# Kernel tuning notes

Measured on AMD Instinct MI355X. Metric: run time of the kernel, lower is better.

Reference implementation:

```python
import jax, jax.numpy as jnp
import numpy as np

BN_EPS = 1e-3  # Keras BatchNormalization default epsilon


def _conv_block(x, k):
    """Per-task conv (stride 2, pad 1) -> ReLU -> BatchNorm (center/scale=False, training).

    x: [B, E, H, W, Cin]  (B tasks, E examples per task)
    k: [B, kh, kw, Cin, Cout]  per-task kernel
    """
    def conv_one(xe, kt):  # xe: [E,H,W,Cin], kt: [kh,kw,Cin,Cout]
        return jax.lax.conv_general_dilated(
            xe, kt, window_strides=(2, 2), padding=[(1, 1), (1, 1)],
            dimension_numbers=('NHWC', 'HWIO', 'NHWC'))
    y = jax.nn.relu(jax.vmap(conv_one)(x, k))  # [B,E,H',W',Cout]
    # BatchNorm in training mode: moments over all axes except channels
    m = jnp.mean(y, axis=(0, 1, 2, 3))
    v = jnp.var(y, axis=(0, 1, 2, 3))
    return (y - m) * jax.lax.rsqrt(v + BN_EPS)


def setup_inputs() -> dict:
    key = jax.random.key(0)
    ks = jax.random.split(key, 6)
    B, E, H, C, O = 64, 64, 28, 64, 20
    return {
        'x': jax.random.normal(ks[0], (B, E, H, H, 1), dtype=jnp.float32),
        'k1': jax.random.normal(ks[1], (B, 3, 3, 1, C), dtype=jnp.float32) * 0.1,
        'k2': jax.random.normal(ks[2], (B, 3, 3, C, C), dtype=jnp.float32) * 0.05,
        'k3': jax.random.normal(ks[3], (B, 3, 3, C, C), dtype=jnp.float32) * 0.05,
        'k4': jax.random.normal(ks[4], (B, 3, 3, C, C), dtype=jnp.float32) * 0.05,
        'w_ro': jax.random.normal(ks[5], (B, C, O), dtype=jnp.float32) * 0.1,
    }


def reference(x, k1, k2, k3, k4, w_ro):
    h = _conv_block(x, k1)   # [B,E,14,14,C]
    h = _conv_block(h, k2)   # [B,E,7,7,C]
    h = _conv_block(h, k3)   # [B,E,4,4,C]
    h = _conv_block(h, k4)   # [B,E,2,2,C]
    # MaxPooling2D with pool size == full spatial extent -> global spatial max
    feat = jnp.max(h, axis=(2, 3))  # [B,E,C]
    # per-task readout matmul: [B,E,H] x [B,H,O] -> [B,E,O]
    return jnp.einsum('beh,bho->beo', feat, w_ro)
```

## Files before the change

kernel.cpp:

```cpp
#include <hip/hip_runtime.h>

#define BN_EPS 1e-3f

typedef __attribute__((ext_vector_type(8))) short bf16x8;
typedef __attribute__((ext_vector_type(16))) float floatx16;
typedef unsigned short u16;

__device__ __forceinline__ u16 f2bf(float f) {
  unsigned u = __float_as_uint(f);
  u += 0x7fffu + ((u >> 16) & 1u);
  return (u16)(u >> 16);
}
__device__ __forceinline__ float bf2f(u16 h) {
  return __uint_as_float(((unsigned)h) << 16);
}

static constexpr int NSHARD = 64;

__global__ __launch_bounds__(256) void prep_k(
    const float* __restrict__ k2, const float* __restrict__ k3,
    const float* __restrict__ k4, u16* __restrict__ k2T,
    u16* __restrict__ k3T, u16* __restrict__ k4T)
{
  __shared__ float T[64 * 68];
  const int blk = blockIdx.x, l = blk >> 6, b = blk & 63;
  const float* src = (l == 0 ? k2 : l == 1 ? k3 : k4) + (size_t)b * 9 * 4096;
  u16* dst = (l == 0 ? k2T : l == 1 ? k3T : k4T) + (size_t)b * 9 * 4096;
  const int tid = threadIdx.x;
  const int cin = tid >> 2, q0 = (tid & 3) * 16;
  const int cout = tid >> 2, ci0 = (tid & 3) * 16;

  for (int s = 0; s < 9; ++s) {
    const float* ss = src + s * 4096;
#pragma unroll
    for (int q = 0; q < 16; q += 4) {
      const float4 v = *(const float4*)(ss + cin * 64 + q0 + q);
      T[(q0 + q + 0) * 68 + cin] = v.x;
      T[(q0 + q + 1) * 68 + cin] = v.y;
      T[(q0 + q + 2) * 68 + cin] = v.z;
      T[(q0 + q + 3) * 68 + cin] = v.w;
    }
    __syncthreads();
    alignas(16) u16 tmp[16];
#pragma unroll
    for (int j = 0; j < 16; ++j) tmp[j] = f2bf(T[cout * 68 + ci0 + j]);
    u16* d = dst + s * 4096 + cout * 64 + ci0;
    *(uint4*)d       = *(uint4*)&tmp[0];
    *(uint4*)(d + 8) = *(uint4*)&tmp[8];
    __syncthreads();
  }
}

__global__ __launch_bounds__(256) void conv1s_k(
    const float* __restrict__ x, const float* __restrict__ k1,
    float* __restrict__ statsSh)
{
  __shared__ float xp[30 * 36];
  __shared__ float w1s[576];
  __shared__ float redsum[64], redss[64];

  const int be = blockIdx.x, b = be >> 6, tid = threadIdx.x;
  const int lane = tid & 63, wave = tid >> 6;
  const int l31 = lane & 31, kq8 = (lane >> 5) * 8;

  for (int i = tid; i < 1080; i += 256) xp[i] = 0.f;
  for (int i = tid; i < 576; i += 256) w1s[i] = k1[(size_t)b * 576 + i];
  if (tid < 64) { redsum[tid] = 0.f; redss[tid] = 0.f; }
  __syncthreads();
  for (int i = tid; i < 784; i += 256) {
    const int r = i / 28, c = i - 28 * r;
    xp[(r + 1) * 36 + (c + 1)] = x[(size_t)be * 784 + i];
  }
  __syncthreads();

  bf16x8 bf0, bf1;
#pragma unroll
  for (int j = 0; j < 8; ++j) {
    const int k = kq8 + j;
    bf0[j] = (k < 9) ? (short)f2bf(w1s[k * 64 + l31]) : (short)0;
    bf1[j] = (k < 9) ? (short)f2bf(w1s[k * 64 + 32 + l31]) : (short)0;
  }

  float s0 = 0.f, q0 = 0.f, s1v = 0.f, q1 = 0.f;
  for (int t = wave; t < 7; t += 4) {
    const int row = t * 32 + l31;
    const int p = row < 196 ? row : 195;
    const int oy = p / 14, ox = p - 14 * oy;
    bf16x8 af;
#pragma unroll
    for (int j = 0; j < 8; ++j) {
      const int k = kq8 + j;
      float v = 0.f;
      if (k < 9) v = xp[(2 * oy + k / 3) * 36 + (2 * ox + k % 3)];
      af[j] = (short)f2bf(v);
    }
    floatx16 z;
#pragma unroll
    for (int r = 0; r < 16; ++r) z[r] = 0.f;
    floatx16 c0 = __builtin_amdgcn_mfma_f32_32x32x16_bf16(af, bf0, z, 0, 0, 0);
    floatx16 c1 = __builtin_amdgcn_mfma_f32_32x32x16_bf16(af, bf1, z, 0, 0, 0);
    const int rb = t * 32 + 4 * (lane >> 5);
#pragma unroll
    for (int r = 0; r < 16; ++r) {
      const int rw = rb + (r & 3) + 8 * (r >> 2);
      if (rw < 196) {
        const float v0 = fmaxf(c0[r], 0.f), v1 = fmaxf(c1[r], 0.f);
        s0 += v0; q0 = fmaf(v0, v0, q0);
        s1v += v1; q1 = fmaf(v1, v1, q1);
      }
    }
  }
  atomicAdd(&redsum[l31], s0);
  atomicAdd(&redss[l31], q0);
  atomicAdd(&redsum[32 + l31], s1v);
  atomicAdd(&redss[32 + l31], q1);
  __syncthreads();
  if (tid < 64) {
    const int sh = be & (NSHARD - 1);
    atomicAdd(&statsSh[sh * 128 + tid], redsum[tid]);
    atomicAdd(&statsSh[sh * 128 + 64 + tid], redss[tid]);
  }
}

__global__ __launch_bounds__(256) void cg2f_k(
    const float* __restrict__ x, const float* __restrict__ k1,
    const u16* __restrict__ k2T, const float* __restrict__ statsPrev,
    float invN, u16* __restrict__ y2, float* __restrict__ statsSh)
{
  __shared__ __align__(16) u16 mapS[225 * 72];
  __shared__ float xp[30 * 36];
  __shared__ float w1s[576];
  __shared__ float P[256];
  __shared__ float s1[64], t1[64];
  __shared__ float redsum[64], redss[64];

  const int be = blockIdx.x, b = be >> 6, tid = threadIdx.x;
  const int lane = tid & 63, wave = tid >> 6;
  const int l31 = lane & 31, kq8 = (lane >> 5) * 8;

  for (int i = tid; i < 1080; i += 256) xp[i] = 0.f;
  for (int i = tid; i < 576; i += 256) w1s[i] = k1[(size_t)b * 576 + i];
  if (tid < 64) { redsum[tid] = 0.f; redss[tid] = 0.f; }
  if (tid < 9) *(uint4*)&mapS[224 * 72 + tid * 8] = uint4{0, 0, 0, 0};
  {
    const int cidx = tid & 127, g = tid >> 7;
    float a = 0.f;
    for (int k = 0; k < NSHARD / 2; ++k)
      a += statsPrev[(g * (NSHARD / 2) + k) * 128 + cidx];
    P[tid] = a;
  }
  __syncthreads();
  if (tid < 64) {
    const float m = (P[tid] + P[tid + 128]) * invN;
    const float var = fmaf(-m, m, (P[64 + tid] + P[192 + tid]) * invN);
    const float s = rsqrtf(var + BN_EPS);
    s1[tid] = s;
    t1[tid] = -m * s;
  }
  for (int i = tid; i < 784; i += 256) {
    const int r = i / 28, c = i - 28 * r;
    xp[(r + 1) * 36 + (c + 1)] = x[(size_t)be * 784 + i];
  }
  __syncthreads();

  {
    bf16x8 bf0, bf1;
#pragma unroll
    for (int j = 0; j < 8; ++j) {
      const int k = kq8 + j;
      bf0[j] = (k < 9) ? (short)f2bf(w1s[k * 64 + l31]) : (short)0;
      bf1[j] = (k < 9) ? (short)f2bf(w1s[k * 64 + 32 + l31]) : (short)0;
    }
    const float sc0 = s1[l31], tc0 = t1[l31];
    const float sc1 = s1[32 + l31], tc1 = t1[32 + l31];
    for (int t = wave; t < 7; t += 4) {
      const int row = t * 32 + l31;
      const int p = row < 196 ? row : 195;
      const int oy = p / 14, ox = p - 14 * oy;
      bf16x8 af;
#pragma unroll
      for (int j = 0; j < 8; ++j) {
        const int k = kq8 + j;
        float v = 0.f;
        if (k < 9) v = xp[(2 * oy + k / 3) * 36 + (2 * ox + k % 3)];
        af[j] = (short)f2bf(v);
      }
      floatx16 z;
#pragma unroll
      for (int r = 0; r < 16; ++r) z[r] = 0.f;
      floatx16 c0 = __builtin_amdgcn_mfma_f32_32x32x16_bf16(af, bf0, z, 0, 0, 0);
      floatx16 c1 = __builtin_amdgcn_mfma_f32_32x32x16_bf16(af, bf1, z, 0, 0, 0);
      const int rb = t * 32 + 4 * (lane >> 5);
#pragma unroll
      for (int r = 0; r < 16; ++r) {
        const int rw = rb + (r & 3) + 8 * (r >> 2);
        mapS[rw * 72 + l31]      = f2bf(fmaf(fmaxf(c0[r], 0.f), sc0, tc0));
        mapS[rw * 72 + 32 + l31] = f2bf(fmaf(fmaxf(c1[r], 0.f), sc1, tc1));
      }
    }
  }
  __syncthreads();

  const int m0 = (wave & 1) * 32, n0 = (wave >> 1) * 32;
  const int lrow = m0 + l31;
  const bool rv = lrow < 49;
  const int oy = rv ? lrow / 7 : 0, ox = rv ? lrow % 7 : 0;
  const u16* wbB = k2T + (size_t)b * 9 * 4096 + (n0 + l31) * 64 + kq8;

  floatx16 acc;
#pragma unroll
  for (int r = 0; r < 16; ++r) acc[r] = 0.f;

#pragma unroll
  for (int s = 0; s < 9; ++s) {
    const int ky = s / 3, kx = s % 3;
    int pix = 224;
    if (rv) {
      const int iy = 2 * oy - 1 + ky, ix = 2 * ox - 1 + kx;
      if ((unsigned)iy < 14u && (unsigned)ix < 14u) pix = iy * 14 + ix;
    }
    const u16* ap = &mapS[pix * 72 + kq8];
    const u16* bp = wbB + s * 4096;
#pragma unroll
    for (int kk = 0; kk < 4; ++kk) {
      bf16x8 a  = *(const bf16x8*)(ap + kk * 16);
      bf16x8 bv = *(const bf16x8*)(bp + kk * 16);
      acc = __builtin_amdgcn_mfma_f32_32x32x16_bf16(a, bv, acc, 0, 0, 0);
    }
  }

  const int col = n0 + l31;
  const int rb = m0 + 4 * (lane >> 5);
  float ls = 0.f, lss = 0.f;
#pragma unroll
  for (int r = 0; r < 16; ++r) {
    const int rw = rb + (r & 3) + 8 * (r >> 2);
    if (rw < 49) {
      const float v = fmaxf(acc[r], 0.f);
      y2[((size_t)be * 49 + rw) * 64 + col] = f2bf(v);
      ls += v;
      lss = fmaf(v, v, lss);
    }
  }
  atomicAdd(&redsum[col], ls);
  atomicAdd(&redss[col], lss);
  __syncthreads();
  if (tid < 64) {
    const int sh = be & (NSHARD - 1);
    atomicAdd(&statsSh[sh * 128 + tid], redsum[tid]);
    atomicAdd(&statsSh[sh * 128 + 64 + tid], redss[tid]);
  }
}

template <int Hin, int Hout, int G>
__device__ __forceinline__ void conv_core_bn(
    const u16* __restrict__ yin, const u16* __restrict__ wT,
    const float* __restrict__ statsPrev, float invN, u16* __restrict__ yout,
    float* __restrict__ statsSh, int blk)
{
  constexpr int PPI  = Hout * Hout;
  constexpr int ROWS = G * PPI;
  constexpr int BPT  = 64 / G;
  constexpr int MR   = G * Hin * Hin;
  constexpr int ZR   = MR;

  __shared__ __align__(16) u16 mapS[(MR + 1) * 72];
  __shared__ float P[256];
  __shared__ float s1[64], t1[64];
  __shared__ float redsum[64], redss[64];

  const int b = blk / BPT, e0 = (blk % BPT) * G;
  const int tid = threadIdx.x, lane = tid & 63, wave = tid >> 6;

  if (tid < 64) { redsum[tid] = 0.f; redss[tid] = 0.f; }
  if (tid < 9) *(uint4*)&mapS[ZR * 72 + tid * 8] = uint4{0, 0, 0, 0};
  {
    const int cidx = tid & 127, g = tid >> 7;
    float a = 0.f;
    for (int k = 0; k < NSHARD / 2; ++k)
      a += statsPrev[(g * (NSHARD / 2) + k) * 128 + cidx];
    P[tid] = a;
  }
  __syncthreads();
  if (tid < 64) {
    const float m = (P[tid] + P[tid + 128]) * invN;
    const float var = fmaf(-m, m, (P[64 + tid] + P[192 + tid]) * invN);
    const float s = rsqrtf(var + BN_EPS);
    s1[tid] = s;
    t1[tid] = -m * s;
  }
  __syncthreads();

  {
    const u16* src = yin + (size_t)(b * 64 + e0) * (Hin * Hin) * 64;
    for (int ch = tid; ch < MR * 8; ch += 256) {
      const int r = ch >> 3, c0 = (ch & 7) * 8;
      uint4 v = *(const uint4*)(src + ch * 8);
      const u16* h = (const u16*)&v;
      alignas(16) u16 o[8];
#pragma unroll
      for (int j = 0; j < 8; ++j)
        o[j] = f2bf(fmaf(bf2f(h[j]), s1[c0 + j], t1[c0 + j]));
      *(uint4*)&mapS[r * 72 + c0] = *(uint4*)o;
    }
  }

  const int m0 = (wave & 1) * 32, n0 = (wave >> 1) * 32;
  const int l31 = lane & 31, kq8 = (lane >> 5) * 8;
  const int lrow = m0 + l31;
  const bool rv = lrow < ROWS;
  const int img = rv ? lrow / PPI : 0;
  const int pp  = rv ? lrow % PPI : 0;
  const int oy = pp / Hout, ox = pp % Hout;
  const u16* wbB = wT + (size_t)b * 9 * 4096 + (n0 + l31) * 64 + kq8;

  floatx16 acc;
#pragma unroll
  for (int r = 0; r < 16; ++r) acc[r] = 0.f;

  __syncthreads();

#pragma unroll
  for (int s = 0; s < 9; ++s) {
    const int ky = s / 3, kx = s % 3;
    int pix = ZR;
    if (rv) {
      const int iy = 2 * oy - 1 + ky, ix = 2 * ox - 1 + kx;
      if ((unsigned)iy < (unsigned)Hin && (unsigned)ix < (unsigned)Hin)
        pix = img * (Hin * Hin) + iy * Hin + ix;
    }
    const u16* ap = &mapS[pix * 72 + kq8];
    const u16* bp = wbB + s * 4096;
#pragma unroll
    for (int kk = 0; kk < 4; ++kk) {
      bf16x8 a  = *(const bf16x8*)(ap + kk * 16);
      bf16x8 bv = *(const bf16x8*)(bp + kk * 16);
      acc = __builtin_amdgcn_mfma_f32_32x32x16_bf16(a, bv, acc, 0, 0, 0);
    }
  }

  const int col = n0 + l31;
  const int rb = m0 + 4 * (lane >> 5);
  float ls = 0.f, lss = 0.f;
#pragma unroll
  for (int r = 0; r < 16; ++r) {
    const int rw = rb + (r & 3) + 8 * (r >> 2);
    if (rw < ROWS) {
      const int re = rw / PPI, pr = rw % PPI;
      const float v = fmaxf(acc[r], 0.f);
      yout[((size_t)(b * 64 + e0 + re) * PPI + pr) * 64 + col] = f2bf(v);
      ls += v;
      lss = fmaf(v, v, lss);
    }
  }
  atomicAdd(&redsum[col], ls);
  atomicAdd(&redss[col], lss);
  __syncthreads();
  if (tid < 64) {
    const int sh = blk & (NSHARD - 1);
    atomicAdd(&statsSh[sh * 128 + tid], redsum[tid]);
    atomicAdd(&statsSh[sh * 128 + 64 + tid], redss[tid]);
  }
}

__global__ __launch_bounds__(256) void cg3_k(
    const u16* __restrict__ yin, const u16* __restrict__ wT,
    const float* __restrict__ stPrev, float invN, u16* __restrict__ yout,
    float* __restrict__ statsSh) {
  conv_core_bn<7, 4, 4>(yin, wT, stPrev, invN, yout, statsSh, blockIdx.x);
}
__global__ __launch_bounds__(256) void cg4_k(
    const u16* __restrict__ yin, const u16* __restrict__ wT,
    const float* __restrict__ stPrev, float invN, u16* __restrict__ yout,
    float* __restrict__ statsSh) {
  conv_core_bn<4, 2, 16>(yin, wT, stPrev, invN, yout, statsSh, blockIdx.x);
}

__global__ __launch_bounds__(256) void readout_k(
    const u16* __restrict__ y4, const float* __restrict__ w_ro,
    const float* __restrict__ statsSh, float invN, float* __restrict__ outp)
{
  __shared__ float wl[64 * 20];
  __shared__ float feat[64 * 64];
  __shared__ float P[256];
  __shared__ float sArr[64], tArr[64];

  const int b = blockIdx.x, tid = threadIdx.x;

  {
    const int g = tid >> 7, cidx = tid & 127;
    float acc = 0.f;
    for (int k = 0; k < NSHARD / 2; ++k)
      acc += statsSh[(g * (NSHARD / 2) + k) * 128 + cidx];
    P[tid] = acc;
  }
  for (int i = tid; i < 1280; i += 256) wl[i] = w_ro[(size_t)b * 1280 + i];
  __syncthreads();
  if (tid < 64) {
    const float m = (P[tid] + P[tid + 128]) * invN;
    const float var = fmaf(-m, m, (P[64 + tid] + P[192 + tid]) * invN);
    const float s = rsqrtf(var + BN_EPS);
    sArr[tid] = s;
    tArr[tid] = -m * s;
  }
  __syncthreads();

  {
    const int e = tid & 63;
    for (int c = tid >> 6; c < 64; c += 4) {
      const u16* p4 = y4 + ((size_t)(b * 64 + e) * 4) * 64 + c;
      const float v = fmaxf(fmaxf(bf2f(p4[0]), bf2f(p4[64])),
                            fmaxf(bf2f(p4[128]), bf2f(p4[192])));
      feat[c * 64 + e] = fmaf(v, sArr[c], tArr[c]);
    }
  }
  __syncthreads();

  const int e = tid >> 2, og = (tid & 3) * 5;
  float acc[5] = {0.f, 0.f, 0.f, 0.f, 0.f};
  for (int c = 0; c < 64; ++c) {
    const float f = feat[c * 64 + e];
#pragma unroll
    for (int j = 0; j < 5; ++j) acc[j] = fmaf(f, wl[c * 20 + og + j], acc[j]);
  }
#pragma unroll
  for (int j = 0; j < 5; ++j)
    outp[((size_t)b * 64 + e) * 20 + og + j] = acc[j];
}

extern "C" void kernel_launch(void* const* d_in, const int* in_sizes, int n_in,
                              void* d_out, int out_size, void* d_ws, size_t ws_size,
                              hipStream_t stream) {
  (void)in_sizes; (void)n_in; (void)out_size; (void)ws_size;
  const float* x   = (const float*)d_in[0];
  const float* k1  = (const float*)d_in[1];
  const float* k2  = (const float*)d_in[2];
  const float* k3  = (const float*)d_in[3];
  const float* k4  = (const float*)d_in[4];
  const float* wro = (const float*)d_in[5];
  float* out = (float*)d_out;
  char* ws = (char*)d_ws;

  float* stats = (float*)ws;
  u16* k2T = (u16*)(ws + 131072);
  u16* k3T = k2T + (size_t)2359296;
  u16* k4T = k3T + (size_t)2359296;
  u16* y2 = k4T + (size_t)2359296;
  u16* y3 = y2 + (size_t)12845056;
  u16* y4 = y3 + (size_t)4194304;

  float* st1 = stats;
  float* st2 = stats + 8192;
  float* st3 = stats + 16384;
  float* st4 = stats + 24576;

  hipMemsetAsync(stats, 0, 131072, stream);

  prep_k<<<192, 256, 0, stream>>>(k2, k3, k4, k2T, k3T, k4T);
  conv1s_k<<<4096, 256, 0, stream>>>(x, k1, st1);
  cg2f_k<<<4096, 256, 0, stream>>>(x, k1, k2T, st1, 1.f / 802816.f, y2, st2);
  cg3_k<<<1024, 256, 0, stream>>>(y2, k3T, st2, 1.f / 200704.f, y3, st3);
  cg4_k<<<256, 256, 0, stream>>>(y3, k4T, st3, 1.f / 65536.f, y4, st4);
  readout_k<<<64, 256, 0, stream>>>(y4, wro, st4, 1.f / 16384.f, out);
}
```

Before: 275.9 us.

## Fold layer-1 BatchNorm into conv2 weights and store raw y1 instead of recomputing

Layer 1 is now computed once. Its raw ReLU output is written to global memory as bf16 and its statistics are gathered in the same pass. A new kernel folds the layer-1 normalization scale into the conv2 weights and builds per-border-class bias terms, so conv2 reads y1 directly and no longer recomputes conv1 per example. Conv2 is restructured to process 4 examples per block with a 256x64 LDS tile. Weight prep for k3/k4 is merged into the layer-1 launch. This trades the duplicated conv1 work for extra global traffic on y1, and the bf16 rounding of scaled weights slightly changes numerics.

```diff
diff --git a/kernel.cpp b/kernel.cpp
--- a/kernel.cpp
+++ b/kernel.cpp
@@ -17,21 +17,149 @@
 
 static constexpr int NSHARD = 64;
 
-__global__ __launch_bounds__(256) void prep_k(
-    const float* __restrict__ k2, const float* __restrict__ k3,
-    const float* __restrict__ k4, u16* __restrict__ k2T,
-    u16* __restrict__ k3T, u16* __restrict__ k4T)
+__global__ __launch_bounds__(256) void c1_k(
+    const float* __restrict__ x, const float* __restrict__ k1,
+    const float* __restrict__ k3, const float* __restrict__ k4,
+    u16* __restrict__ k3T, u16* __restrict__ k4T,
+    u16* __restrict__ y1, float* __restrict__ statsSh)
+{
+  __shared__ __align__(16) char lds[17408];
+  const int tid = threadIdx.x;
+
+  if (blockIdx.x >= 4096) {
+    float* T = (float*)lds;
+    const int blk = blockIdx.x - 4096, l = blk >> 6, b = blk & 63;
+    const float* src = (l == 0 ? k3 : k4) + (size_t)b * 9 * 4096;
+    u16* dst = (l == 0 ? k3T : k4T) + (size_t)b * 9 * 4096;
+    const int cin = tid >> 2, q0 = (tid & 3) * 16;
+    const int cout = tid >> 2, ci0 = (tid & 3) * 16;
+    for (int s = 0; s < 9; ++s) {
+      const float* ss = src + s * 4096;
+#pragma unroll
+      for (int q = 0; q < 16; q += 4) {
+        const float4 v = *(const float4*)(ss + cin * 64 + q0 + q);
+        T[(q0 + q + 0) * 68 + cin] = v.x;
+        T[(q0 + q + 1) * 68 + cin] = v.y;
+        T[(q0 + q + 2) * 68 + cin] = v.z;
+        T[(q0 + q + 3) * 68 + cin] = v.w;
+      }
+      __syncthreads();
+      alignas(16) u16 tmp[16];
+#pragma unroll
+      for (int j = 0; j < 16; ++j) tmp[j] = f2bf(T[cout * 68 + ci0 + j]);
+      u16* d = dst + s * 4096 + cout * 64 + ci0;
+      *(uint4*)d       = *(uint4*)&tmp[0];
+      *(uint4*)(d + 8) = *(uint4*)&tmp[8];
+      __syncthreads();
+    }
+    return;
+  }
+
+  float* xp     = (float*)lds;
+  float* w1s    = (float*)(lds + 4320);
+  float* redsum = (float*)(lds + 6624);
+  float* redss  = (float*)(lds + 6880);
+
+  const int be = blockIdx.x, b = be >> 6;
+  const int lane = tid & 63, wave = tid >> 6;
+  const int l31 = lane & 31, kq8 = (lane >> 5) * 8;
+
+  for (int i = tid; i < 1080; i += 256) xp[i] = 0.f;
+  for (int i = tid; i < 576; i += 256) w1s[i] = k1[(size_t)b * 576 + i];
+  if (tid < 64) { redsum[tid] = 0.f; redss[tid] = 0.f; }
+  __syncthreads();
+  for (int i = tid; i < 784; i += 256) {
+    const int r = i / 28, c = i - 28 * r;
+    xp[(r + 1) * 36 + (c + 1)] = x[(size_t)be * 784 + i];
+  }
+  __syncthreads();
+
+  bf16x8 bf0, bf1;
+#pragma unroll
+  for (int j = 0; j < 8; ++j) {
+    const int k = kq8 + j;
+    bf0[j] = (k < 9) ? (short)f2bf(w1s[k * 64 + l31]) : (short)0;
+    bf1[j] = (k < 9) ? (short)f2bf(w1s[k * 64 + 32 + l31]) : (short)0;
+  }
+
+  float s0 = 0.f, q0v = 0.f, s1v = 0.f, q1v = 0.f;
+  for (int t = wave; t < 7; t += 4) {
+    const int row = t * 32 + l31;
+    const int p = row < 196 ? row : 195;
+    const int oy = p / 14, ox = p - 14 * oy;
+    bf16x8 af;
+#pragma unroll
+    for (int j = 0; j < 8; ++j) {
+      const int k = kq8 + j;
+      float v = 0.f;
+      if (k < 9) v = xp[(2 * oy + k / 3) * 36 + (2 * ox + k % 3)];
+      af[j] = (short)f2bf(v);
+    }
+    floatx16 z;
+#pragma unroll
+    for (int r = 0; r < 16; ++r) z[r] = 0.f;
+    floatx16 c0 = __builtin_amdgcn_mfma_f32_32x32x16_bf16(af, bf0, z, 0, 0, 0);
+    floatx16 c1 = __builtin_amdgcn_mfma_f32_32x32x16_bf16(af, bf1, z, 0, 0, 0);
+    const int rb = t * 32 + 4 * (lane >> 5);
+#pragma unroll
+    for (int r = 0; r < 16; ++r) {
+      const int rw = rb + (r & 3) + 8 * (r >> 2);
+      if (rw < 196) {
+        const float v0 = fmaxf(c0[r], 0.f), v1 = fmaxf(c1[r], 0.f);
+        const size_t ob = ((size_t)be * 196 + rw) * 64;
+        y1[ob + l31]      = f2bf(v0);
+        y1[ob + 32 + l31] = f2bf(v1);
+        s0 += v0;  q0v = fmaf(v0, v0, q0v);
+        s1v += v1; q1v = fmaf(v1, v1, q1v);
+      }
+    }
+  }
+  atomicAdd(&redsum[l31], s0);
+  atomicAdd(&redss[l31], q0v);
+  atomicAdd(&redsum[32 + l31], s1v);
+  atomicAdd(&redss[32 + l31], q1v);
+  __syncthreads();
+  if (tid < 64) {
+    const int sh = be & (NSHARD - 1);
+    atomicAdd(&statsSh[sh * 128 + tid], redsum[tid]);
+    atomicAdd(&statsSh[sh * 128 + 64 + tid], redss[tid]);
+  }
+}
+
+__global__ __launch_bounds__(256) void foldw_k(
+    const float* __restrict__ W, const float* __restrict__ statsSh, float invN,
+    u16* __restrict__ Wf, float* __restrict__ biasCls)
 {
   __shared__ float T[64 * 68];
-  const int blk = blockIdx.x, l = blk >> 6, b = blk & 63;
-  const float* src = (l == 0 ? k2 : l == 1 ? k3 : k4) + (size_t)b * 9 * 4096;
-  u16* dst = (l == 0 ? k2T : l == 1 ? k3T : k4T) + (size_t)b * 9 * 4096;
+  __shared__ float P[256];
+  __shared__ float s1[64], t1[64];
+  __shared__ float tbS[64];
+
+  const int b = blockIdx.x / 3, sg = blockIdx.x % 3;
   const int tid = threadIdx.x;
+
+  {
+    const int g = tid >> 7, cidx = tid & 127;
+    float acc = 0.f;
+    for (int k = 0; k < NSHARD / 2; ++k)
+      acc += statsSh[(g * (NSHARD / 2) + k) * 128 + cidx];
+    P[tid] = acc;
+  }
+  __syncthreads();
+  if (tid < 64) {
+    const float m = (P[tid] + P[tid + 128]) * invN;
+    const float var = fmaf(-m, m, (P[64 + tid] + P[192 + tid]) * invN);
+    const float s = rsqrtf(var + BN_EPS);
+    s1[tid] = s;
+    t1[tid] = -m * s;
+  }
+  __syncthreads();
+
   const int cin = tid >> 2, q0 = (tid & 3) * 16;
   const int cout = tid >> 2, ci0 = (tid & 3) * 16;
-
-  for (int s = 0; s < 9; ++s) {
-    const float* ss = src + s * 4096;
+  for (int s = sg * 3; s < sg * 3 + 3; ++s) {
+    if (tid < 64) tbS[tid] = 0.f;
+    const float* ss = W + ((size_t)b * 9 + s) * 4096;
 #pragma unroll
     for (int q = 0; q < 16; q += 4) {
       const float4 v = *(const float4*)(ss + cin * 64 + q0 + q);
@@ -42,211 +170,131 @@
     }
     __syncthreads();
     alignas(16) u16 tmp[16];
-#pragma unroll
-    for (int j = 0; j < 16; ++j) tmp[j] = f2bf(T[cout * 68 + ci0 + j]);
-    u16* d = dst + s * 4096 + cout * 64 + ci0;
-    *(uint4*)d       = *(uint4*)&tmp[0];
-    *(uint4*)(d + 8) = *(uint4*)&tmp[8];
+    float tb = 0.f;
+#pragma unroll
+    for (int j = 0; j < 16; ++j) {
+      const float wv = T[cout * 68 + ci0 + j];
+      tmp[j] = f2bf(wv * s1[ci0 + j]);
+      tb = fmaf(t1[ci0 + j], wv, tb);
+    }
+    u16* dst = Wf + ((size_t)b * 9 + s) * 4096 + cout * 64 + ci0;
+    *(uint4*)dst       = *(uint4*)&tmp[0];
+    *(uint4*)(dst + 8) = *(uint4*)&tmp[8];
+    atomicAdd(&tbS[cout], tb);
     __syncthreads();
-  }
-}
-
-__global__ __launch_bounds__(256) void conv1s_k(
-    const float* __restrict__ x, const float* __restrict__ k1,
+    if (tid < 64) {
+      const int ky = s / 3, kx = s % 3;
+      const float tv = tbS[tid];
+#pragma unroll
+      for (int cls = 0; cls < 9; ++cls) {
+        const int ry = cls / 3, rx = cls % 3;
+        const bool valid = !((ry == 1 && ky == 0) || (ry == 2 && ky == 2) ||
+                             (rx == 1 && kx == 0) || (rx == 2 && kx == 2));
+        if (valid) atomicAdd(&biasCls[(size_t)b * 576 + cls * 64 + tid], tv);
+      }
+    }
+    __syncthreads();
+  }
+}
+
+__global__ __launch_bounds__(256) void cg2_k(
+    const u16* __restrict__ y1, const u16* __restrict__ k2f,
+    const float* __restrict__ biasCls, u16* __restrict__ y2,
     float* __restrict__ statsSh)
 {
-  __shared__ float xp[30 * 36];
-  __shared__ float w1s[576];
+  __shared__ __align__(16) u16 AS[256 * 72];
+  __shared__ __align__(16) u16 BtS[64 * 72];
+  __shared__ float biasS[576];
   __shared__ float redsum[64], redss[64];
 
-  const int be = blockIdx.x, b = be >> 6, tid = threadIdx.x;
-  const int lane = tid & 63, wave = tid >> 6;
+  const int b = blockIdx.x >> 4, e0 = (blockIdx.x & 15) * 4;
+  const int tid = threadIdx.x, lane = tid & 63, wave = tid >> 6;
   const int l31 = lane & 31, kq8 = (lane >> 5) * 8;
 
-  for (int i = tid; i < 1080; i += 256) xp[i] = 0.f;
-  for (int i = tid; i < 576; i += 256) w1s[i] = k1[(size_t)b * 576 + i];
+  for (int i = tid; i < 576; i += 256) biasS[i] = biasCls[(size_t)b * 576 + i];
   if (tid < 64) { redsum[tid] = 0.f; redss[tid] = 0.f; }
-  __syncthreads();
-  for (int i = tid; i < 784; i += 256) {
-    const int r = i / 28, c = i - 28 * r;
-    xp[(r + 1) * 36 + (c + 1)] = x[(size_t)be * 784 + i];
-  }
-  __syncthreads();
-
-  bf16x8 bf0, bf1;
-#pragma unroll
-  for (int j = 0; j < 8; ++j) {
-    const int k = kq8 + j;
-    bf0[j] = (k < 9) ? (short)f2bf(w1s[k * 64 + l31]) : (short)0;
-    bf1[j] = (k < 9) ? (short)f2bf(w1s[k * 64 + 32 + l31]) : (short)0;
-  }
-
-  float s0 = 0.f, q0 = 0.f, s1v = 0.f, q1 = 0.f;
-  for (int t = wave; t < 7; t += 4) {
-    const int row = t * 32 + l31;
-    const int p = row < 196 ? row : 195;
-    const int oy = p / 14, ox = p - 14 * oy;
-    bf16x8 af;
-#pragma unroll
-    for (int j = 0; j < 8; ++j) {
-      const int k = kq8 + j;
-      float v = 0.f;
-      if (k < 9) v = xp[(2 * oy + k / 3) * 36 + (2 * ox + k % 3)];
-      af[j] = (short)f2bf(v);
-    }
-    floatx16 z;
-#pragma unroll
-    for (int r = 0; r < 16; ++r) z[r] = 0.f;
-    floatx16 c0 = __builtin_amdgcn_mfma_f32_32x32x16_bf16(af, bf0, z, 0, 0, 0);
-    floatx16 c1 = __builtin_amdgcn_mfma_f32_32x32x16_bf16(af, bf1, z, 0, 0, 0);
-    const int rb = t * 32 + 4 * (lane >> 5);
-#pragma unroll
-    for (int r = 0; r < 16; ++r) {
-      const int rw = rb + (r & 3) + 8 * (r >> 2);
-      if (rw < 196) {
-        const float v0 = fmaxf(c0[r], 0.f), v1 = fmaxf(c1[r], 0.f);
-        s0 += v0; q0 = fmaf(v0, v0, q0);
-        s1v += v1; q1 = fmaf(v1, v1, q1);
-      }
-    }
-  }
-  atomicAdd(&redsum[l31], s0);
-  atomicAdd(&redss[l31], q0);
-  atomicAdd(&redsum[32 + l31], s1v);
-  atomicAdd(&redss[32 + l31], q1);
-  __syncthreads();
-  if (tid < 64) {
-    const int sh = be & (NSHARD - 1);
-    atomicAdd(&statsSh[sh * 128 + tid], redsum[tid]);
-    atomicAdd(&statsSh[sh * 128 + 64 + tid], redss[tid]);
-  }
-}
-
-__global__ __launch_bounds__(256) void cg2f_k(
-    const float* __restrict__ x, const float* __restrict__ k1,
-    const u16* __restrict__ k2T, const float* __restrict__ statsPrev,
-    float invN, u16* __restrict__ y2, float* __restrict__ statsSh)
-{
-  __shared__ __align__(16) u16 mapS[225 * 72];
-  __shared__ float xp[30 * 36];
-  __shared__ float w1s[576];
-  __shared__ float P[256];
-  __shared__ float s1[64], t1[64];
-  __shared__ float redsum[64], redss[64];
-
-  const int be = blockIdx.x, b = be >> 6, tid = threadIdx.x;
-  const int lane = tid & 63, wave = tid >> 6;
-  const int l31 = lane & 31, kq8 = (lane >> 5) * 8;
-
-  for (int i = tid; i < 1080; i += 256) xp[i] = 0.f;
-  for (int i = tid; i < 576; i += 256) w1s[i] = k1[(size_t)b * 576 + i];
-  if (tid < 64) { redsum[tid] = 0.f; redss[tid] = 0.f; }
-  if (tid < 9) *(uint4*)&mapS[224 * 72 + tid * 8] = uint4{0, 0, 0, 0};
-  {
-    const int cidx = tid & 127, g = tid >> 7;
-    float a = 0.f;
-    for (int k = 0; k < NSHARD / 2; ++k)
-      a += statsPrev[(g * (NSHARD / 2) + k) * 128 + cidx];
-    P[tid] = a;
-  }
-  __syncthreads();
-  if (tid < 64) {
-    const float m = (P[tid] + P[tid + 128]) * invN;
-    const float var = fmaf(-m, m, (P[64 + tid] + P[192 + tid]) * invN);
-    const float s = rsqrtf(var + BN_EPS);
-    s1[tid] = s;
-    t1[tid] = -m * s;
-  }
-  for (int i = tid; i < 784; i += 256) {
-    const int r = i / 28, c = i - 28 * r;
-    xp[(r + 1) * 36 + (c + 1)] = x[(size_t)be * 784 + i];
-  }
-  __syncthreads();
-
-  {
-    bf16x8 bf0, bf1;
-#pragma unroll
-    for (int j = 0; j < 8; ++j) {
-      const int k = kq8 + j;
-      bf0[j] = (k < 9) ? (short)f2bf(w1s[k * 64 + l31]) : (short)0;
-      bf1[j] = (k < 9) ? (short)f2bf(w1s[k * 64 + 32 + l31]) : (short)0;
-    }
-    const float sc0 = s1[l31], tc0 = t1[l31];
-    const float sc1 = s1[32 + l31], tc1 = t1[32 + l31];
-    for (int t = wave; t < 7; t += 4) {
-      const int row = t * 32 + l31;
-      const int p = row < 196 ? row : 195;
-      const int oy = p / 14, ox = p - 14 * oy;
-      bf16x8 af;
-#pragma unroll
-      for (int j = 0; j < 8; ++j) {
-        const int k = kq8 + j;
-        float v = 0.f;
-        if (k < 9) v = xp[(2 * oy + k / 3) * 36 + (2 * ox + k % 3)];
-        af[j] = (short)f2bf(v);
-      }
-      floatx16 z;
-#pragma unroll
-      for (int r = 0; r < 16; ++r) z[r] = 0.f;
-      floatx16 c0 = __builtin_amdgcn_mfma_f32_32x32x16_bf16(af, bf0, z, 0, 0, 0);
-      floatx16 c1 = __builtin_amdgcn_mfma_f32_32x32x16_bf16(af, bf1, z, 0, 0, 0);
-      const int rb = t * 32 + 4 * (lane >> 5);
-#pragma unroll
-      for (int r = 0; r < 16; ++r) {
-        const int rw = rb + (r & 3) + 8 * (r >> 2);
-        mapS[rw * 72 + l31]      = f2bf(fmaf(fmaxf(c0[r], 0.f), sc0, tc0));
-        mapS[rw * 72 + 32 + l31] = f2bf(fmaf(fmaxf(c1[r], 0.f), sc1, tc1));
-      }
-    }
-  }
-  __syncthreads();
-
-  const int m0 = (wave & 1) * 32, n0 = (wave >> 1) * 32;
-  const int lrow = m0 + l31;
-  const bool rv = lrow < 49;
-  const int oy = rv ? lrow / 7 : 0, ox = rv ? lrow % 7 : 0;
-  const u16* wbB = k2T + (size_t)b * 9 * 4096 + (n0 + l31) * 64 + kq8;
-
-  floatx16 acc;
-#pragma unroll
-  for (int r = 0; r < 16; ++r) acc[r] = 0.f;
-
-#pragma unroll
+  for (int i = tid; i < 480; i += 256) {
+    const int row = 196 + (i >> 3), c8 = (i & 7) * 8;
+    *(uint4*)&AS[row * 72 + c8] = uint4{0, 0, 0, 0};
+  }
+
+  const size_t yb = (size_t)(b * 64 + e0) * 196 * 64;
+  const u16* wb = k2f + (size_t)b * 9 * 4096;
+  const int bco = tid >> 2, bci = (tid & 3) * 16;
+  const int m0 = wave * 64;
+
+  floatx16 acc00, acc01, acc10, acc11;
+#pragma unroll
+  for (int r = 0; r < 16; ++r) {
+    acc00[r] = 0.f; acc01[r] = 0.f; acc10[r] = 0.f; acc11[r] = 0.f;
+  }
+
   for (int s = 0; s < 9; ++s) {
     const int ky = s / 3, kx = s % 3;
-    int pix = 224;
-    if (rv) {
+    for (int i = tid; i < 1568; i += 256) {
+      const int row = i >> 3, c8 = (i & 7) * 8;
+      const int e_l = row / 49, pp = row % 49;
+      const int oy = pp / 7, ox = pp % 7;
       const int iy = 2 * oy - 1 + ky, ix = 2 * ox - 1 + kx;
-      if ((unsigned)iy < 14u && (unsigned)ix < 14u) pix = iy * 14 + ix;
-    }
-    const u16* ap = &mapS[pix * 72 + kq8];
-    const u16* bp = wbB + s * 4096;
+      uint4 v = uint4{0, 0, 0, 0};
+      if ((unsigned)iy < 14u && (unsigned)ix < 14u)
+        v = *(const uint4*)(y1 + yb + ((size_t)e_l * 196 + iy * 14 + ix) * 64 + c8);
+      *(uint4*)&AS[row * 72 + c8] = v;
+    }
+    {
+      const u16* g = wb + s * 4096 + bco * 64 + bci;
+      *(uint4*)&BtS[bco * 72 + bci]     = *(const uint4*)g;
+      *(uint4*)&BtS[bco * 72 + bci + 8] = *(const uint4*)(g + 8);
+    }
+    __syncthreads();
 #pragma unroll
     for (int kk = 0; kk < 4; ++kk) {
-      bf16x8 a  = *(const bf16x8*)(ap + kk * 16);
-      bf16x8 bv = *(const bf16x8*)(bp + kk * 16);
-      acc = __builtin_amdgcn_mfma_f32_32x32x16_bf16(a, bv, acc, 0, 0, 0);
-    }
-  }
-
-  const int col = n0 + l31;
-  const int rb = m0 + 4 * (lane >> 5);
-  float ls = 0.f, lss = 0.f;
-#pragma unroll
-  for (int r = 0; r < 16; ++r) {
-    const int rw = rb + (r & 3) + 8 * (r >> 2);
-    if (rw < 49) {
-      const float v = fmaxf(acc[r], 0.f);
-      y2[((size_t)be * 49 + rw) * 64 + col] = f2bf(v);
-      ls += v;
-      lss = fmaf(v, v, lss);
-    }
-  }
-  atomicAdd(&redsum[col], ls);
-  atomicAdd(&redss[col], lss);
+      const int ko = kk * 16 + kq8;
+      bf16x8 a0 = *(const bf16x8*)&AS[(m0 + l31) * 72 + ko];
+      bf16x8 a1 = *(const bf16x8*)&AS[(m0 + 32 + l31) * 72 + ko];
+      bf16x8 b0 = *(const bf16x8*)&BtS[l31 * 72 + ko];
+      bf16x8 b1 = *(const bf16x8*)&BtS[(32 + l31) * 72 + ko];
+      acc00 = __builtin_amdgcn_mfma_f32_32x32x16_bf16(a0, b0, acc00, 0, 0, 0);
+      acc01 = __builtin_amdgcn_mfma_f32_32x32x16_bf16(a0, b1, acc01, 0, 0, 0);
+      acc10 = __builtin_amdgcn_mfma_f32_32x32x16_bf16(a1, b0, acc10, 0, 0, 0);
+      acc11 = __builtin_amdgcn_mfma_f32_32x32x16_bf16(a1, b1, acc11, 0, 0, 0);
+    }
+    __syncthreads();
+  }
+
+  float ls0 = 0.f, lss0 = 0.f, ls1 = 0.f, lss1 = 0.f;
+  const int col0 = l31, col1 = 32 + l31;
+#pragma unroll
+  for (int mt = 0; mt < 2; ++mt) {
+    const floatx16& aN0 = mt ? acc10 : acc00;
+    const floatx16& aN1 = mt ? acc11 : acc01;
+    const int rbb = m0 + mt * 32 + 4 * (lane >> 5);
+#pragma unroll
+    for (int r = 0; r < 16; ++r) {
+      const int rw = rbb + (r & 3) + 8 * (r >> 2);
+      if (rw < 196) {
+        const int e_l = rw / 49, pr = rw % 49;
+        const int ooy = pr / 7, oox = pr % 7;
+        const int ry = (ooy == 0) ? 1 : 0;
+        const int rx = (oox == 0) ? 1 : 0;
+        const int cls = ry * 3 + rx;
+        const size_t ob = ((size_t)(b * 64 + e0 + e_l) * 49 + pr) * 64;
+        const float v0 = fmaxf(aN0[r] + biasS[cls * 64 + col0], 0.f);
+        const float v1 = fmaxf(aN1[r] + biasS[cls * 64 + col1], 0.f);
+        y2[ob + col0] = f2bf(v0);
+        y2[ob + col1] = f2bf(v1);
+        ls0 += v0; lss0 = fmaf(v0, v0, lss0);
+        ls1 += v1; lss1 = fmaf(v1, v1, lss1);
+      }
+    }
+  }
+  atomicAdd(&redsum[col0], ls0);
+  atomicAdd(&redss[col0], lss0);
+  atomicAdd(&redsum[col1], ls1);
+  atomicAdd(&redss[col1], lss1);
   __syncthreads();
   if (tid < 64) {
-    const int sh = be & (NSHARD - 1);
+    const int sh = blockIdx.x & (NSHARD - 1);
     atomicAdd(&statsSh[sh * 128 + tid], redsum[tid]);
     atomicAdd(&statsSh[sh * 128 + 64 + tid], redss[tid]);
   }
@@ -442,23 +490,25 @@
   char* ws = (char*)d_ws;
 
   float* stats = (float*)ws;
-  u16* k2T = (u16*)(ws + 131072);
-  u16* k3T = k2T + (size_t)2359296;
-  u16* k4T = k3T + (size_t)2359296;
-  u16* y2 = k4T + (size_t)2359296;
-  u16* y3 = y2 + (size_t)12845056;
-  u16* y4 = y3 + (size_t)4194304;
+  float* bias2 = (float*)(ws + 131072);
+  u16* k2f = (u16*)(ws + 278528);
+  u16* k3T = (u16*)(ws + 4997120);
+  u16* k4T = (u16*)(ws + 9715712);
+  u16* y2  = (u16*)(ws + 14434304);
+  u16* y1  = (u16*)(ws + 40124416);
+  u16* y3  = y1;
+  u16* y4  = y3 + (size_t)4194304;
 
   float* st1 = stats;
   float* st2 = stats + 8192;
   float* st3 = stats + 16384;
   float* st4 = stats + 24576;
 
-  hipMemsetAsync(stats, 0, 131072, stream);
-
-  prep_k<<<192, 256, 0, stream>>>(k2, k3, k4, k2T, k3T, k4T);
-  conv1s_k<<<4096, 256, 0, stream>>>(x, k1, st1);
-  cg2f_k<<<4096, 256, 0, stream>>>(x, k1, k2T, st1, 1.f / 802816.f, y2, st2);
+  hipMemsetAsync(stats, 0, 131072 + 147456, stream);
+
+  c1_k<<<4224, 256, 0, stream>>>(x, k1, k3, k4, k3T, k4T, y1, st1);
+  foldw_k<<<192, 256, 0, stream>>>(k2, st1, 1.f / 802816.f, k2f, bias2);
+  cg2_k<<<1024, 256, 0, stream>>>(y1, k2f, bias2, y2, st2);
   cg3_k<<<1024, 256, 0, stream>>>(y2, k3T, st2, 1.f / 200704.f, y3, st3);
   cg4_k<<<256, 256, 0, stream>>>(y3, k4T, st3, 1.f / 65536.f, y4, st4);
   readout_k<<<64, 256, 0, stream>>>(y4, wro, st4, 1.f / 16384.f, out);
```

Measured after the change: 268.7 us. 2.6% less time.
